# Performance work log

Measured on AMD Instinct MI355X. Metric: run time of the kernel, lower is better.

## Reference

```python
import jax, jax.numpy as jnp
import numpy as np

D = 2048; HQ = 16; HKV = 4; HD = 128
E = 8; F = 2048; FS = 11008; TOPK = 2
B = 2; S = 1024
EPS = 1e-6
NEG = -1e9


def setup_inputs() -> dict:
    key = jax.random.key(0)
    ks = jax.random.split(key, 16)
    p = lambda k, shape: jax.random.normal(k, shape, jnp.float32) * 0.02
    # rotary tables (rotate-half convention): [S, HD]
    pos = jnp.arange(S, dtype=jnp.float32)[:, None]
    inv = 1.0 / (10000.0 ** (jnp.arange(0, HD, 2, dtype=jnp.float32) / HD))
    ang = pos * inv[None, :]
    cos = jnp.concatenate([jnp.cos(ang), jnp.cos(ang)], axis=-1)
    sin = jnp.concatenate([jnp.sin(ang), jnp.sin(ang)], axis=-1)
    return dict(
        x=jax.random.normal(ks[0], (B, S, D), jnp.float32),
        rope_cos=cos, rope_sin=sin,
        attn_norm_w=jnp.ones((D,), jnp.float32),
        ffn_norm_w=jnp.ones((D,), jnp.float32),
        wq=p(ks[1], (D, HQ * HD)), bq=jnp.zeros((HQ * HD,), jnp.float32),
        wk=p(ks[2], (D, HKV * HD)), bk=jnp.zeros((HKV * HD,), jnp.float32),
        wv=p(ks[3], (D, HKV * HD)), bv=jnp.zeros((HKV * HD,), jnp.float32),
        wo=p(ks[4], (HQ * HD, D)),
        router_w=p(ks[5], (D, E)),
        w_gate=p(ks[6], (E, D, F)), w_up=p(ks[7], (E, D, F)), w_down=p(ks[8], (E, F, D)),
        ws_gate=p(ks[9], (D, FS)), ws_up=p(ks[10], (D, FS)), ws_down=p(ks[11], (FS, D)),
    )


def rmsnorm(x, w):
    return x * jax.lax.rsqrt(jnp.mean(x * x, axis=-1, keepdims=True) + EPS) * w


def rotate_half(x):
    x1, x2 = jnp.split(x, 2, axis=-1)
    return jnp.concatenate([-x2, x1], axis=-1)


def reference(x, rope_cos, rope_sin, attn_norm_w, ffn_norm_w,
              wq, bq, wk, bk, wv, bv, wo, router_w,
              w_gate, w_up, w_down, ws_gate, ws_up, ws_down):
    b, s, d = x.shape
    # ---- attention sublayer ----
    h = rmsnorm(x, attn_norm_w)
    q = (h @ wq + bq).reshape(b, s, HQ, HD)
    k = (h @ wk + bk).reshape(b, s, HKV, HD)
    v = (h @ wv + bv).reshape(b, s, HKV, HD)
    cos = rope_cos[None, :, None, :]
    sin = rope_sin[None, :, None, :]
    q = q * cos + rotate_half(q) * sin
    k = k * cos + rotate_half(k) * sin
    rep = HQ // HKV
    k = jnp.repeat(k, rep, axis=2)   # [b,s,HQ,HD]
    v = jnp.repeat(v, rep, axis=2)
    scores = jnp.einsum('bqhd,bkhd->bhqk', q, k) / np.sqrt(HD).astype(np.float32)
    causal = jnp.tril(jnp.ones((s, s), bool))
    scores = jnp.where(causal[None, None], scores, NEG)
    attn = jax.nn.softmax(scores, axis=-1)
    o = jnp.einsum('bhqk,bkhd->bqhd', attn, v).reshape(b, s, HQ * HD) @ wo
    new_k, new_v = k, v
    x = x + o
    # ---- MoE sublayer ----
    hn = rmsnorm(x, ffn_norm_w).reshape(b * s, d)   # [T,D]
    logits = hn @ router_w                           # [T,E]
    probs = jax.nn.softmax(logits, axis=-1)
    topv, topi = jax.lax.top_k(probs, TOPK)          # [T,K]
    topv = topv / jnp.sum(topv, axis=-1, keepdims=True)
    onehot = jax.nn.one_hot(topi, E, dtype=hn.dtype)  # [T,K,E]
    wdense = jnp.einsum('tke,tk->te', onehot, topv)   # sparse combine weights [T,E]
    g = jnp.einsum('td,edf->tef', hn, w_gate)
    u = jnp.einsum('td,edf->tef', hn, w_up)
    y = jnp.einsum('tef,efd->ted', jax.nn.silu(g) * u, w_down)
    routed = jnp.einsum('ted,te->td', y, wdense)
    shared = (jax.nn.silu(hn @ ws_gate) * (hn @ ws_up)) @ ws_down
    moe = (routed + shared).reshape(b, s, d)
    # load-balancing aux loss (Switch/Mixtral convention)
    frac = jnp.mean(onehot, axis=(0, 1))             # fraction dispatched per expert
    pmean = jnp.mean(probs, axis=0)
    aux_loss = E * jnp.sum(frac * pmean)
    out = x + moe
    return out, (new_k, new_v), aux_loss
```

## Files before the change

### kernel.cpp

```cpp
#include <hip/hip_runtime.h>

typedef unsigned short u16;
typedef unsigned int u32;
typedef unsigned long long u64;
typedef __attribute__((ext_vector_type(4))) unsigned short u16x4;
typedef __attribute__((ext_vector_type(8))) unsigned short u16x8;
typedef __attribute__((ext_vector_type(4))) float f32x4;
typedef __attribute__((ext_vector_type(8))) __bf16 bf16x8;

#define DD 2048
#define TT 2048
#define FSH 11008

__device__ __forceinline__ float bf2f(u16 u) {
  union { u32 i; float f; } v; v.i = ((u32)u) << 16; return v.f;
}
__device__ __forceinline__ u16 f2bf(float f) {
  union { float f; u32 i; } v; v.f = f;
  u32 r = v.i + 0x7fffu + ((v.i >> 16) & 1u);
  return (u16)(r >> 16);
}
__device__ __forceinline__ void gld16(const void* g, void* l) {
  __builtin_amdgcn_global_load_lds((const __attribute__((address_space(1))) void*)g,
                                   (__attribute__((address_space(3))) void*)l, 16, 0, 0);
}

#define MFMA16(d, a, b) d = __builtin_amdgcn_mfma_f32_16x16x32_bf16(a, b, d, 0, 0, 0)

__global__ __launch_bounds__(256) void rmsnorm_k(const float* __restrict__ x,
                                                 const float* __restrict__ w,
                                                 u16* __restrict__ out) {
  const int t = threadIdx.x;
  const float* xr = x + (size_t)blockIdx.x * DD;
  float4 a = *(const float4*)(xr + t * 8);
  float4 b = *(const float4*)(xr + t * 8 + 4);
  float ss = a.x*a.x + a.y*a.y + a.z*a.z + a.w*a.w
           + b.x*b.x + b.y*b.y + b.z*b.z + b.w*b.w;
#pragma unroll
  for (int m = 1; m < 64; m <<= 1) ss += __shfl_xor(ss, m);
  __shared__ float red[4];
  if ((t & 63) == 0) red[t >> 6] = ss;
  __syncthreads();
  float sc = rsqrtf((red[0] + red[1] + red[2] + red[3]) * (1.f / DD) + 1e-6f);
  float4 wa = *(const float4*)(w + t * 8);
  float4 wb = *(const float4*)(w + t * 8 + 4);
  u16x8 o;
  o[0] = f2bf(a.x * sc * wa.x); o[1] = f2bf(a.y * sc * wa.y);
  o[2] = f2bf(a.z * sc * wa.z); o[3] = f2bf(a.w * sc * wa.w);
  o[4] = f2bf(b.x * sc * wb.x); o[5] = f2bf(b.y * sc * wb.y);
  o[6] = f2bf(b.z * sc * wb.z); o[7] = f2bf(b.w * sc * wb.w);
  *(u16x8*)(out + (size_t)blockIdx.x * DD + t * 8) = o;
}

__global__ __launch_bounds__(256) void transp_k(const float* __restrict__ W,
                                                u16* __restrict__ Wt, int R, int C) {
  __shared__ u16 tile[64 * 80];
  const size_t msz = (size_t)R * C;
  const float* Wm = W + msz * blockIdx.z;
  u16* Wtm = Wt + msz * blockIdx.z;
  const int t = threadIdx.x;
  const int n0 = blockIdx.x * 64, k0 = blockIdx.y * 64;
#pragma unroll
  for (int p = 0; p < 4; ++p) {
    const int kk = (t >> 4) + p * 16;
    const int nn = (t & 15) * 4;
    float4 v = *(const float4*)(Wm + (size_t)(k0 + kk) * C + n0 + nn);
    const float vv[4] = {v.x, v.y, v.z, v.w};
#pragma unroll
    for (int j = 0; j < 4; ++j) {
      const int n = nn + j;
      tile[n * 80 + (kk ^ (((n >> 2) & 7) << 3))] = f2bf(vv[j]);
    }
  }
  __syncthreads();
#pragma unroll
  for (int p = 0; p < 2; ++p) {
    const int n = (t >> 3) + p * 32;
    const int c = t & 7;
    u16x8 v = *(const u16x8*)(tile + n * 80 + ((c * 8) ^ (((n >> 2) & 7) << 3)));
    *(u16x8*)(Wtm + (size_t)(n0 + n) * R + k0 + c * 8) = v;
  }
}

template <int EPI, bool EXPERT, bool INDIR, bool SPLITK>
__global__ __launch_bounds__(256) void gemm2(
    const u16* __restrict__ A, const u16* __restrict__ Bt, void* __restrict__ Cp,
    const void* __restrict__ aux, const float* __restrict__ slotw,
    const int* __restrict__ slot_tok, const int* __restrict__ tiletab,
    int M, int N, int K, int Kc) {
  __shared__ u16 lA[128 * 32];
  __shared__ u16 lB[128 * 32];
  const int t = threadIdx.x, w = t >> 6, l = t & 63;
  const int n0 = blockIdx.x * 128;
  int m0;
  if constexpr (EXPERT) {
    const int ntil = tiletab[0];
    if ((int)blockIdx.y >= ntil) return;
    const int e = tiletab[1 + blockIdx.y * 2];
    m0 = tiletab[2 + blockIdx.y * 2];
    Bt += (size_t)e * N * K;
  } else {
    m0 = blockIdx.y * 128;
  }
  int kbase = 0, KC = K;
  if constexpr (SPLITK) { kbase = blockIdx.z * Kc; KC = Kc; }
  const int srow = w * 16 + (l >> 2);
  const int scol = (l & 3) * 8;
  const int r0 = m0 + srow, r1 = m0 + srow + 64;
  const u16 *ag0, *ag1;
  if constexpr (INDIR) {
    ag0 = A + (size_t)slot_tok[r0] * K + scol + kbase;
    ag1 = A + (size_t)slot_tok[r1] * K + scol + kbase;
  } else {
    ag0 = A + (size_t)r0 * K + scol + kbase;
    ag1 = A + (size_t)r1 * K + scol + kbase;
  }
  const u16* bg0 = Bt + (size_t)(n0 + srow) * K + scol + kbase;
  const u16* bg1 = Bt + (size_t)(n0 + srow + 64) * K + scol + kbase;
  u16* la = lA + w * 512;
  u16* lb = lB + w * 512;
  const int l15 = l & 15, l4 = l >> 4;
  const int wm = w >> 1, wn = w & 1;
  const int fa = (wm * 64 + l15) * 32 + l4 * 8;
  const int fb = (wn * 64 + l15) * 32 + l4 * 8;
  f32x4 acc[4][4] = {};
  for (int ko = 0; ko < KC; ko += 32) {
    __syncthreads();
    gld16(ag0 + ko, la);
    gld16(ag1 + ko, la + 2048);
    gld16(bg0 + ko, lb);
    gld16(bg1 + ko, lb + 2048);
    asm volatile("s_waitcnt vmcnt(0)" ::: "memory");
    __syncthreads();
    bf16x8 af[4], bf[4];
#pragma unroll
    for (int i = 0; i < 4; ++i) {
      af[i] = *(const bf16x8*)(lA + fa + i * 512);
      bf[i] = *(const bf16x8*)(lB + fb + i * 512);
    }
#pragma unroll
    for (int mi = 0; mi < 4; ++mi)
#pragma unroll
      for (int ni = 0; ni < 4; ++ni)
        MFMA16(acc[mi][ni], af[mi], bf[ni]);
  }
  float* Cf = (float*)Cp;
  if constexpr (SPLITK) Cf += (size_t)blockIdx.z * M * N;
#pragma unroll
  for (int mi = 0; mi < 4; ++mi) {
#pragma unroll
    for (int r = 0; r < 4; ++r) {
      const int row = m0 + wm * 64 + mi * 16 + l4 * 4 + r;
#pragma unroll
      for (int ni = 0; ni < 4; ++ni) {
        const int col = n0 + wn * 64 + ni * 16 + l15;
        const size_t idx = (size_t)row * N + col;
        const float v = acc[mi][ni][r];
        if constexpr (EPI == 0) Cf[idx] = v;
        else if constexpr (EPI == 2) ((u16*)Cp)[idx] = f2bf(v);
        else if constexpr (EPI == 3) {
          const float g = bf2f(((const u16*)aux)[idx]);
          ((u16*)Cp)[idx] = f2bf(v * g / (1.f + __expf(-g)));
        } else {
          ((u16*)Cp)[idx] = f2bf(slotw[row] * v);
        }
      }
    }
  }
}

__global__ __launch_bounds__(512) void gemm2gu(
    const u16* __restrict__ A, const u16* __restrict__ Btg, const u16* __restrict__ Btu,
    u16* __restrict__ act, const int* __restrict__ slot_tok, const int* __restrict__ tiletab,
    int N, int K, int ebase) {
  __shared__ u16 SH[16384];
  const int t = threadIdx.x, w = t >> 6, l = t & 63;
  const int n0 = blockIdx.x * 128;
  const int ntil = tiletab[0];
  if ((int)blockIdx.y >= ntil) return;
  const int e = tiletab[1 + blockIdx.y * 2];
  if (e < ebase || e >= ebase + 4) return;
  const int m0 = tiletab[2 + blockIdx.y * 2];
  const size_t boff = (size_t)(e - ebase) * N * K;
  const u16* Bg = Btg + boff;
  const u16* Bu = Btu + boff;
  const int srow = w * 16 + (l >> 2);
  const int scol = (l & 3) * 8;
  const u16* ag = A + (size_t)slot_tok[m0 + srow] * K + scol;
  const u16* bgp = Bg + (size_t)(n0 + srow) * K + scol;
  const u16* bup = Bu + (size_t)(n0 + srow) * K + scol;
  u16* la = SH + w * 512;
  u16* lbg = SH + 4096 + w * 512;
  u16* lbu = SH + 8192 + w * 512;
  const int l15 = l & 15, l4 = l >> 4;
  const int wm = w >> 2, wn = w & 3;
  const int mat = wn >> 1, ch = wn & 1;
  const int fa = (wm * 64 + l15) * 32 + l4 * 8;
  const int fb = (mat ? 8192 : 4096) + (ch * 64 + l15) * 32 + l4 * 8;
  f32x4 acc[4][4] = {};
  for (int ko = 0; ko < K; ko += 32) {
    __syncthreads();
    gld16(ag + ko, la);
    gld16(bgp + ko, lbg);
    gld16(bup + ko, lbu);
    asm volatile("s_waitcnt vmcnt(0)" ::: "memory");
    __syncthreads();
    bf16x8 af[4], bf[4];
#pragma unroll
    for (int i = 0; i < 4; ++i) {
      af[i] = *(const bf16x8*)(SH + fa + i * 512);
      bf[i] = *(const bf16x8*)(SH + fb + i * 512);
    }
#pragma unroll
    for (int mi = 0; mi < 4; ++mi)
#pragma unroll
      for (int ni = 0; ni < 4; ++ni)
        MFMA16(acc[mi][ni], af[mi], bf[ni]);
  }
  __syncthreads();
  if (mat == 0) {
    u16* gr = SH + (wm * 2 + ch) * 4096;
#pragma unroll
    for (int mi = 0; mi < 4; ++mi)
#pragma unroll
      for (int r = 0; r < 4; ++r)
#pragma unroll
        for (int ni = 0; ni < 4; ++ni)
          gr[(mi * 16 + l4 * 4 + r) * 64 + ni * 16 + l15] = f2bf(acc[mi][ni][r]);
  }
  __syncthreads();
  if (mat == 1) {
    const u16* gr = SH + (wm * 2 + ch) * 4096;
#pragma unroll
    for (int mi = 0; mi < 4; ++mi)
#pragma unroll
      for (int r = 0; r < 4; ++r) {
        const int row = m0 + wm * 64 + mi * 16 + l4 * 4 + r;
#pragma unroll
        for (int ni = 0; ni < 4; ++ni) {
          const float g = bf2f(gr[(mi * 16 + l4 * 4 + r) * 64 + ni * 16 + l15]);
          const float u = acc[mi][ni][r];
          act[(size_t)row * N + n0 + ch * 64 + ni * 16 + l15] =
              f2bf(u * g / (1.f + __expf(-g)));
        }
      }
  }
}

template <int EPI, bool SPLITK>
__global__ __launch_bounds__(512, 2) void gemm8(
    const u16* __restrict__ A, const u16* __restrict__ Bt, void* __restrict__ Cp,
    const u16* __restrict__ aux, int M, int N, int K, int Kc) {
  __shared__ char lds[131072];
  const int t = threadIdx.x, w = t >> 6, l = t & 63;
  const int gx = gridDim.x, gy = gridDim.y;
  const int nwg = gx * gy;
  int wg = blockIdx.y * gx + blockIdx.x;
  wg = (wg & 7) * (nwg >> 3) + (wg >> 3);
  const int m0 = (wg % gy) * 256;
  const int n0 = (wg / gy) * 256;
  int kbase = 0, KC = K;
  if constexpr (SPLITK) {
    kbase = blockIdx.z * Kc;
    const int rem = K - kbase;
    KC = rem < Kc ? rem : Kc;
  }
  const int ktiles = KC >> 6;
  const int wm = w >> 2, wn = w & 3;
  const int l15 = l & 15, l4 = l >> 4;
  const int sro = l >> 3, sc = l & 7;

  const u16* sgp[2][2][2];
  u32 sdo[2][2][2];
#pragma unroll
  for (int isB = 0; isB < 2; ++isB)
#pragma unroll
    for (int h = 0; h < 2; ++h)
#pragma unroll
      for (int i = 0; i < 2; ++i) {
        const int q = i * 8 + w;
        const int r0 = isB ? (((q >> 2) << 6) + h * 32 + (q & 3) * 8)
                           : (((q & 8) << 4) + h * 64 + (q & 7) * 8);
        const int r = r0 + sro;
        const int cl = sc ^ (r & 7);
        const u16* base = isB ? (Bt + (size_t)(n0 + r) * K) : (A + (size_t)(m0 + r) * K);
        sgp[isB][h][i] = base + kbase + cl * 8;
        sdo[isB][h][i] = (u32)(isB * 32768 + r0 * 128);
      }
  auto stage = [&](int b, int isB, int h, int kt) {
    const int kk = kt < ktiles ? kt : ktiles - 1;
#pragma unroll
    for (int i = 0; i < 2; ++i)
      gld16(sgp[isB][h][i] + kk * 64, lds + b * 65536 + sdo[isB][h][i]);
  };
  auto ldA = [&](int b, int mi, int ks) {
    const int row = wm * 128 + mi * 16 + l15;
    const int ch = (ks * 4 + l4) ^ (row & 7);
    return *(const bf16x8*)(lds + b * 65536 + row * 128 + ch * 16);
  };
  auto ldB = [&](int b, int ni, int ks) {
    const int row = wn * 64 + ni * 16 + l15;
    const int ch = (ks * 4 + l4) ^ (row & 7);
    return *(const bf16x8*)(lds + b * 65536 + 32768 + row * 128 + ch * 16);
  };

  f32x4 acc[8][4] = {};
  bf16x8 aR[4][2], b0[2][2], b1[2][2];

  stage(0, 0, 0, 0); stage(0, 1, 0, 0); stage(0, 1, 1, 0); stage(0, 0, 1, 0);
  stage(1, 0, 0, 1); stage(1, 1, 1, 1); stage(1, 0, 1, 1);
  asm volatile("s_waitcnt vmcnt(6)" ::: "memory");
  __builtin_amdgcn_s_barrier();

  for (int kt = 0; kt < ktiles; kt += 2) {
#pragma unroll
    for (int mi = 0; mi < 4; ++mi) { aR[mi][0] = ldA(0, mi, 0); aR[mi][1] = ldA(0, mi, 1); }
#pragma unroll
    for (int ni = 0; ni < 2; ++ni) { b0[ni][0] = ldB(0, ni, 0); b0[ni][1] = ldB(0, ni, 1); }
    stage(1, 1, 0, kt + 1);
    __builtin_amdgcn_s_barrier();
    asm volatile("s_waitcnt lgkmcnt(0)" ::: "memory");
    __builtin_amdgcn_s_setprio(1);
#pragma unroll
    for (int mi = 0; mi < 4; ++mi)
#pragma unroll
      for (int ni = 0; ni < 2; ++ni) {
        MFMA16(acc[mi][ni], aR[mi][0], b0[ni][0]);
        MFMA16(acc[mi][ni], aR[mi][1], b0[ni][1]);
      }
    __builtin_amdgcn_s_setprio(0);
    __builtin_amdgcn_s_barrier();
#pragma unroll
    for (int ni = 0; ni < 2; ++ni) { b1[ni][0] = ldB(0, ni + 2, 0); b1[ni][1] = ldB(0, ni + 2, 1); }
    stage(0, 0, 0, kt + 2);
    __builtin_amdgcn_s_barrier();
    asm volatile("s_waitcnt lgkmcnt(0)" ::: "memory");
    __builtin_amdgcn_s_setprio(1);
#pragma unroll
    for (int mi = 0; mi < 4; ++mi)
#pragma unroll
      for (int ni = 0; ni < 2; ++ni) {
        MFMA16(acc[mi][ni + 2], aR[mi][0], b1[ni][0]);
        MFMA16(acc[mi][ni + 2], aR[mi][1], b1[ni][1]);
// ... 29 lines not shown
    asm volatile("s_waitcnt vmcnt(6)" ::: "memory");
    __builtin_amdgcn_s_barrier();
#pragma unroll
    for (int mi = 0; mi < 4; ++mi) { aR[mi][0] = ldA(1, mi, 0); aR[mi][1] = ldA(1, mi, 1); }
#pragma unroll
    for (int ni = 0; ni < 2; ++ni) { b0[ni][0] = ldB(1, ni, 0); b0[ni][1] = ldB(1, ni, 1); }
    stage(0, 1, 0, kt + 2);
    __builtin_amdgcn_s_barrier();
    asm volatile("s_waitcnt lgkmcnt(0)" ::: "memory");
    __builtin_amdgcn_s_setprio(1);
#pragma unroll
    for (int mi = 0; mi < 4; ++mi)
#pragma unroll
      for (int ni = 0; ni < 2; ++ni) {
        MFMA16(acc[mi][ni], aR[mi][0], b0[ni][0]);
        MFMA16(acc[mi][ni], aR[mi][1], b0[ni][1]);
      }
    __builtin_amdgcn_s_setprio(0);
    __builtin_amdgcn_s_barrier();
#pragma unroll
    for (int ni = 0; ni < 2; ++ni) { b1[ni][0] = ldB(1, ni + 2, 0); b1[ni][1] = ldB(1, ni + 2, 1); }
    stage(1, 0, 0, kt + 3);
    __builtin_amdgcn_s_barrier();
    asm volatile("s_waitcnt lgkmcnt(0)" ::: "memory");
    __builtin_amdgcn_s_setprio(1);
#pragma unroll
    for (int mi = 0; mi < 4; ++mi)
#pragma unroll
      for (int ni = 0; ni < 2; ++ni) {
        MFMA16(acc[mi][ni + 2], aR[mi][0], b1[ni][0]);
        MFMA16(acc[mi][ni + 2], aR[mi][1], b1[ni][1]);
      }
    __builtin_amdgcn_s_setprio(0);
    __builtin_amdgcn_s_barrier();
#pragma unroll
    for (int mi = 0; mi < 4; ++mi) { aR[mi][0] = ldA(1, mi + 4, 0); aR[mi][1] = ldA(1, mi + 4, 1); }
    stage(1, 1, 1, kt + 3);
    __builtin_amdgcn_s_barrier();
    asm volatile("s_waitcnt lgkmcnt(0)" ::: "memory");
    __builtin_amdgcn_s_setprio(1);
#pragma unroll
    for (int mi = 0; mi < 4; ++mi)
#pragma unroll
      for (int ni = 0; ni < 2; ++ni) {
        MFMA16(acc[mi + 4][ni + 2], aR[mi][0], b1[ni][0]);
        MFMA16(acc[mi + 4][ni + 2], aR[mi][1], b1[ni][1]);
      }
    __builtin_amdgcn_s_setprio(0);
    __builtin_amdgcn_s_barrier();
    stage(1, 0, 1, kt + 3);
    __builtin_amdgcn_s_barrier();
    __builtin_amdgcn_s_setprio(1);
#pragma unroll
    for (int mi = 0; mi < 4; ++mi)
#pragma unroll
      for (int ni = 0; ni < 2; ++ni) {
        MFMA16(acc[mi + 4][ni], aR[mi][0], b0[ni][0]);
        MFMA16(acc[mi + 4][ni], aR[mi][1], b0[ni][1]);
      }
    __builtin_amdgcn_s_setprio(0);
    asm volatile("s_waitcnt vmcnt(6)" ::: "memory");
    __builtin_amdgcn_s_barrier();
  }

  u16* C16 = (u16*)Cp;
  float* Cf = (float*)Cp;
  if constexpr (EPI == 10) C16 += (size_t)blockIdx.z * ((size_t)M * N);
  if constexpr (EPI == 11) Cf += (size_t)blockIdx.z * ((size_t)M * N);
#pragma unroll
  for (int mi = 0; mi < 8; ++mi)
#pragma unroll
    for (int rr = 0; rr < 4; ++rr) {
      const int row = m0 + wm * 128 + mi * 16 + l4 * 4 + rr;
#pragma unroll
      for (int ni = 0; ni < 4; ++ni) {
        const int col = n0 + wn * 64 + ni * 16 + l15;
        const size_t idx = (size_t)row * N + col;
        const float v = acc[mi][ni][rr];
        if constexpr (EPI == 11) {
          Cf[idx] = v;
        } else if constexpr (EPI == 3) {
          const float g = bf2f(aux[idx]);
          C16[idx] = f2bf(v * g / (1.f + __expf(-g)));
        } else {
          C16[idx] = f2bf(v);
        }
      }
    }
}

__global__ __launch_bounds__(512, 2) void gemm_gu(
    const u16* __restrict__ A, const u16* __restrict__ Btg, const u16* __restrict__ Btu,
    u16* __restrict__ act, int K, int LDC, int cg0) {
  __shared__ char lds[131072];
  const int t = threadIdx.x, w = t >> 6, l = t & 63;
  const int gx = gridDim.x;
  const int nwg = gx * 8;
  int wg = blockIdx.y * gx + blockIdx.x;
  wg = (wg & 7) * (nwg >> 3) + (wg >> 3);
  const int m0 = (wg & 7) * 256;
  const int nt = wg >> 3;
  const int ktiles = K >> 6;
  const int wm = w >> 2, wn = w & 3;
  const int l15 = l & 15, l4 = l >> 4;
  const int sro = l >> 3, sc = l & 7;

  const u16* sga[2][2]; u32 sda[2][2];
#pragma unroll
  for (int h = 0; h < 2; ++h)
#pragma unroll
    for (int i = 0; i < 2; ++i) {
      const int q = i * 8 + w;
      const int r0 = ((q & 8) << 4) + h * 64 + (q & 7) * 8;
      const int r = r0 + sro;
      const int cl = sc ^ (r & 7);
      sga[h][i] = A + (size_t)(m0 + r) * K + cl * 8;
      sda[h][i] = (u32)(r0 * 128);
    }
  const u16* sgb[2][2]; u32 sdb[2][2];
#pragma unroll
  for (int mat = 0; mat < 2; ++mat)
#pragma unroll
    for (int i = 0; i < 2; ++i) {
      const int q = i * 8 + w;
      const int r0 = q * 8;
      const int r = r0 + sro;
      const int cl = sc ^ (r & 7);
      const u16* B = mat ? Btu : Btg;
      sgb[mat][i] = B + (size_t)(nt * 128 + r) * K + cl * 8;
      sdb[mat][i] = (u32)(32768 + mat * 16384 + r0 * 128);
    }
  auto stgA = [&](int b, int h, int kt) {
    const int kk = kt < ktiles ? kt : ktiles - 1;
#pragma unroll
    for (int i = 0; i < 2; ++i) gld16(sga[h][i] + kk * 64, lds + b * 65536 + sda[h][i]);
  };
  auto stgB = [&](int b, int mat, int kt) {
    const int kk = kt < ktiles ? kt : ktiles - 1;
#pragma unroll
    for (int i = 0; i < 2; ++i) gld16(sgb[mat][i] + kk * 64, lds + b * 65536 + sdb[mat][i]);
  };
  auto ldA = [&](int b, int mi, int ks) {
    const int row = wm * 128 + mi * 16 + l15;
    const int ch = (ks * 4 + l4) ^ (row & 7);
    return *(const bf16x8*)(lds + b * 65536 + row * 128 + ch * 16);
  };
  auto ldB = [&](int b, int mat, int ni, int ks) {
    const int row = wn * 32 + ni * 16 + l15;
    const int ch = (ks * 4 + l4) ^ (row & 7);
    return *(const bf16x8*)(lds + b * 65536 + 32768 + mat * 16384 + row * 128 + ch * 16);
  };

  f32x4 accg[8][2] = {}, accu[8][2] = {};
  bf16x8 aR[4][2], bg[2][2], bu[2][2];

  stgA(0, 0, 0); stgB(0, 0, 0); stgB(0, 1, 0); stgA(0, 1, 0);
  stgA(1, 0, 1); stgB(1, 1, 1); stgA(1, 1, 1);
  asm volatile("s_waitcnt vmcnt(6)" ::: "memory");
  __builtin_amdgcn_s_barrier();

  for (int kt = 0; kt < ktiles; kt += 2) {
#pragma unroll
    for (int mi = 0; mi < 4; ++mi) { aR[mi][0] = ldA(0, mi, 0); aR[mi][1] = ldA(0, mi, 1); }
#pragma unroll
    for (int ni = 0; ni < 2; ++ni) { bg[ni][0] = ldB(0, 0, ni, 0); bg[ni][1] = ldB(0, 0, ni, 1); }
    stgB(1, 0, kt + 1);
    __builtin_amdgcn_s_barrier();
    asm volatile("s_waitcnt lgkmcnt(0)" ::: "memory");
    __builtin_amdgcn_s_setprio(1);
#pragma unroll
    for (int mi = 0; mi < 4; ++mi)
#pragma unroll
      for (int ni = 0; ni < 2; ++ni) {
        MFMA16(accg[mi][ni], aR[mi][0], bg[ni][0]);
        MFMA16(accg[mi][ni], aR[mi][1], bg[ni][1]);
      }
    __builtin_amdgcn_s_setprio(0);
    __builtin_amdgcn_s_barrier();
#pragma unroll
    for (int ni = 0; ni < 2; ++ni) { bu[ni][0] = ldB(0, 1, ni, 0); bu[ni][1] = ldB(0, 1, ni, 1); }
    stgA(0, 0, kt + 2);
    __builtin_amdgcn_s_barrier();
    asm volatile("s_waitcnt lgkmcnt(0)" ::: "memory");
    __builtin_amdgcn_s_setprio(1);
#pragma unroll
    for (int mi = 0; mi < 4; ++mi)
#pragma unroll
      for (int ni = 0; ni < 2; ++ni) {
        MFMA16(accu[mi][ni], aR[mi][0], bu[ni][0]);
        MFMA16(accu[mi][ni], aR[mi][1], bu[ni][1]);
      }
    __builtin_amdgcn_s_setprio(0);
    __builtin_amdgcn_s_barrier();
#pragma unroll
    for (int mi = 0; mi < 4; ++mi) { aR[mi][0] = ldA(0, mi + 4, 0); aR[mi][1] = ldA(0, mi + 4, 1); }
    stgB(0, 1, kt + 2);
    __builtin_amdgcn_s_barrier();
    asm volatile("s_waitcnt lgkmcnt(0)" ::: "memory");
    __builtin_amdgcn_s_setprio(1);
#pragma unroll
    for (int mi = 0; mi < 4; ++mi)
#pragma unroll
      for (int ni = 0; ni < 2; ++ni) {
        MFMA16(accu[mi + 4][ni], aR[mi][0], bu[ni][0]);
        MFMA16(accu[mi + 4][ni], aR[mi][1], bu[ni][1]);
      }
    __builtin_amdgcn_s_setprio(0);
    __builtin_amdgcn_s_barrier();
    stgA(0, 1, kt + 2);
    __builtin_amdgcn_s_barrier();
    __builtin_amdgcn_s_setprio(1);
// ... 288 lines not shown
  const size_t base = (size_t)tok * DD + t * 8;
  float v[8];
  {
    float4 a = *(const float4*)(x + base);
    float4 b = *(const float4*)(x + base + 4);
    v[0] = a.x; v[1] = a.y; v[2] = a.z; v[3] = a.w;
    v[4] = b.x; v[5] = b.y; v[6] = b.z; v[7] = b.w;
  }
#pragma unroll
  for (int p = 0; p < 4; ++p) {
    const float* pr = parts + (size_t)p * (TT * DD) + base;
    float4 a = *(const float4*)(pr);
    float4 b = *(const float4*)(pr + 4);
    v[0] += a.x; v[1] += a.y; v[2] += a.z; v[3] += a.w;
    v[4] += b.x; v[5] += b.y; v[6] += b.z; v[7] += b.w;
  }
  *(float4*)(X2 + base) = make_float4(v[0], v[1], v[2], v[3]);
  *(float4*)(X2 + base + 4) = make_float4(v[4], v[5], v[6], v[7]);
  float ss = 0.f;
#pragma unroll
  for (int j = 0; j < 8; ++j) ss += v[j] * v[j];
#pragma unroll
  for (int m = 1; m < 64; m <<= 1) ss += __shfl_xor(ss, m);
  __shared__ float red[4];
  __shared__ float racc[32];
  if ((t & 63) == 0) red[w] = ss;
  __syncthreads();
  const float sc = rsqrtf((red[0] + red[1] + red[2] + red[3]) * (1.f / DD) + 1e-6f);
  float hn[8];
  u16x8 o;
#pragma unroll
  for (int j = 0; j < 8; ++j) {
    hn[j] = v[j] * sc * wn[t * 8 + j];
    o[j] = f2bf(hn[j]);
  }
  *(u16x8*)(HN + base) = o;
  float acc[8] = {};
#pragma unroll
  for (int j = 0; j < 8; ++j) {
    const int d = t * 8 + j;
    float4 r0 = *(const float4*)(rw + d * 8);
    float4 r1 = *(const float4*)(rw + d * 8 + 4);
    acc[0] += hn[j] * r0.x; acc[1] += hn[j] * r0.y; acc[2] += hn[j] * r0.z; acc[3] += hn[j] * r0.w;
    acc[4] += hn[j] * r1.x; acc[5] += hn[j] * r1.y; acc[6] += hn[j] * r1.z; acc[7] += hn[j] * r1.w;
  }
#pragma unroll
  for (int m = 1; m < 64; m <<= 1)
#pragma unroll
    for (int e = 0; e < 8; ++e) acc[e] += __shfl_xor(acc[e], m);
  if ((t & 63) == 0)
#pragma unroll
    for (int e = 0; e < 8; ++e) racc[w * 8 + e] = acc[e];
  __syncthreads();
  if (t == 0) {
    float lg[8];
#pragma unroll
    for (int e = 0; e < 8; ++e) lg[e] = racc[e] + racc[8 + e] + racc[16 + e] + racc[24 + e];
    float mx = lg[0];
#pragma unroll
    for (int e = 1; e < 8; ++e) mx = fmaxf(mx, lg[e]);
    float p[8], sum = 0.f;
#pragma unroll
    for (int e = 0; e < 8; ++e) { p[e] = __expf(lg[e] - mx); sum += p[e]; }
    const float inv = 1.f / sum;
#pragma unroll
    for (int e = 0; e < 8; ++e) p[e] *= inv;
    *(float4*)(probs + tok * 8) = make_float4(p[0], p[1], p[2], p[3]);
    *(float4*)(probs + tok * 8 + 4) = make_float4(p[4], p[5], p[6], p[7]);
    int e0 = 0; float v0 = p[0];
#pragma unroll
    for (int e = 1; e < 8; ++e) if (p[e] > v0) { v0 = p[e]; e0 = e; }
    int e1 = (e0 == 0) ? 1 : 0; float v1 = p[e1];
#pragma unroll
    for (int e = 0; e < 8; ++e) if (e != e0 && p[e] > v1) { v1 = p[e]; e1 = e; }
    const float wsum = v0 + v1;
    topi2[tok * 2] = e0; topi2[tok * 2 + 1] = e1;
    topw2[tok * 2] = v0 / wsum; topw2[tok * 2 + 1] = v1 / wsum;
  }
}

__global__ __launch_bounds__(256) void zero_k(int* __restrict__ slot_tok,
                                              float* __restrict__ slot_w) {
  const int i = blockIdx.x * 256 + threadIdx.x;
  if (i < 5120) { slot_tok[i] = 0; slot_w[i] = 0.f; }
}

__global__ __launch_bounds__(256) void scan2_k(const int* __restrict__ topi2,
                                               const float* __restrict__ probs,
                                               int* __restrict__ cursors,
                                               int* __restrict__ tiletab,
                                               float* __restrict__ auxout) {
  const int t = threadIdx.x, w = t >> 6, l = t & 63;
  __shared__ int cnt[8];
  __shared__ float wsum[4][8];
  if (t < 8) cnt[t] = 0;
  __syncthreads();
  float ps[8] = {};
  for (int i = t; i < 2048; i += 256) {
    atomicAdd(&cnt[topi2[i * 2]], 1);
    atomicAdd(&cnt[topi2[i * 2 + 1]], 1);
    float4 a = *(const float4*)(probs + i * 8);
    float4 b = *(const float4*)(probs + i * 8 + 4);
    ps[0] += a.x; ps[1] += a.y; ps[2] += a.z; ps[3] += a.w;
    ps[4] += b.x; ps[5] += b.y; ps[6] += b.z; ps[7] += b.w;
  }
#pragma unroll
  for (int m = 1; m < 64; m <<= 1)
#pragma unroll
    for (int e = 0; e < 8; ++e) ps[e] += __shfl_xor(ps[e], m);
  if (l == 0)
#pragma unroll
    for (int e = 0; e < 8; ++e) wsum[w][e] = ps[e];
  __syncthreads();
  if (t == 0) {
    int off = 0, nt = 0;
    float aux = 0.f;
    for (int e = 0; e < 8; ++e) {
      cursors[e] = off;
      const int c = cnt[e];
      const int nte = (c + 127) >> 7;
      for (int i = 0; i < nte; ++i) {
        tiletab[1 + nt * 2] = e;
        tiletab[2 + nt * 2] = off + i * 128;
        ++nt;
      }
      off += nte * 128;
      const float pm = (wsum[0][e] + wsum[1][e] + wsum[2][e] + wsum[3][e]) * (1.f / 2048.f);
      aux += ((float)c * (1.f / 4096.f)) * pm;
    }
    tiletab[0] = nt;
    *auxout = 8.f * aux;
  }
}

__global__ __launch_bounds__(256) void assign_k(const int* __restrict__ topi2,
                                                const float* __restrict__ topw2,
                                                int* __restrict__ cursors,
                                                int* __restrict__ slot_tok,
                                                float* __restrict__ slot_w,
                                                int* __restrict__ tok_slot) {
  __shared__ int lcnt[8];
  __shared__ int base[8];
  const int t = threadIdx.x;
  const int tok = blockIdx.x * 256 + t;
  if (t < 8) lcnt[t] = 0;
  __syncthreads();
  int e[2], lr[2];
#pragma unroll
  for (int j = 0; j < 2; ++j) {
    e[j] = topi2[tok * 2 + j];
    lr[j] = atomicAdd(&lcnt[e[j]], 1);
  }
  __syncthreads();
  if (t < 8) base[t] = atomicAdd(&cursors[t], lcnt[t]);
  __syncthreads();
#pragma unroll
  for (int j = 0; j < 2; ++j) {
    const int s = base[e[j]] + lr[j];
    slot_tok[s] = tok;
    slot_w[s] = topw2[tok * 2 + j];
    tok_slot[tok * 2 + j] = s;
  }
}

__global__ __launch_bounds__(256) void final_k(float* __restrict__ out,
                                               const u16* __restrict__ routed,
                                               const int* __restrict__ tok_slot) {
  const int tok = blockIdx.x, t = threadIdx.x;
  const int s0 = tok_slot[tok * 2], s1 = tok_slot[tok * 2 + 1];
  u16x8 a = ((const u16x8*)(routed + (size_t)s0 * DD))[t];
  u16x8 b = ((const u16x8*)(routed + (size_t)s1 * DD))[t];
  float* o = out + (size_t)tok * DD + t * 8;
  float4 o0 = *(const float4*)o;
  float4 o1 = *(const float4*)(o + 4);
  o0.x += bf2f(a[0]) + bf2f(b[0]); o0.y += bf2f(a[1]) + bf2f(b[1]);
  o0.z += bf2f(a[2]) + bf2f(b[2]); o0.w += bf2f(a[3]) + bf2f(b[3]);
  o1.x += bf2f(a[4]) + bf2f(b[4]); o1.y += bf2f(a[5]) + bf2f(b[5]);
  o1.z += bf2f(a[6]) + bf2f(b[6]); o1.w += bf2f(a[7]) + bf2f(b[7]);
  *(float4*)o = o0;
  *(float4*)(o + 4) = o1;
}

extern "C" void kernel_launch(void* const* d_in, const int* in_sizes, int n_in,
                              void* d_out, int out_size, void* d_ws, size_t ws_size,
                              hipStream_t stream) {
  (void)in_sizes; (void)n_in; (void)out_size; (void)ws_size;
  const float* x    = (const float*)d_in[0];
  const float* rc   = (const float*)d_in[1];
  const float* rs   = (const float*)d_in[2];
  const float* anw  = (const float*)d_in[3];
  const float* fnw  = (const float*)d_in[4];
  const float* wq   = (const float*)d_in[5];
  const float* bq   = (const float*)d_in[6];
  const float* wk   = (const float*)d_in[7];
  const float* bk   = (const float*)d_in[8];
  const float* wv   = (const float*)d_in[9];
  const float* bv   = (const float*)d_in[10];
  const float* wo   = (const float*)d_in[11];
  const float* rw   = (const float*)d_in[12];
  const float* wg   = (const float*)d_in[13];
  const float* wu   = (const float*)d_in[14];
  const float* wd   = (const float*)d_in[15];
  const float* wsg  = (const float*)d_in[16];
  const float* wsu  = (const float*)d_in[17];
  const float* wsd  = (const float*)d_in[18];

  const size_t MB = (size_t)1 << 20;
  char* ws = (char*)d_ws;
  float* X2  = (float*)(ws + 0);
  u16*   HN  = (u16*)(ws + 16 * MB);
  char*  SM  = ws + 24 * MB;
  char*  AR  = ws + 25 * MB;

  int*   CURS  = (int*)(SM + 256);
  int*   TILT  = (int*)(SM + 512);
  int*   TOPI  = (int*)(SM + 4096);
  float* TOPW  = (float*)(SM + 40960);
  int*   STOK  = (int*)(SM + 73728);
  float* SW    = (float*)(SM + 98304);
  int*   TSLOT = (int*)(SM + 131072);
  float* PROBS = (float*)(SM + 163840);

  u16*   H      = (u16*)(AR);
  u16*   WTQ    = (u16*)(AR + 8 * MB);
  u16*   PARTSQ = (u16*)(AR + 20 * MB);
  u16*   ATTNO = (u16*)(AR);
  u16*   QR    = (u16*)(AR + 68 * MB);
  u16*   KR    = (u16*)(AR + 76 * MB);
  u16*   VBb   = (u16*)(AR + 78 * MB);
  u16*   WTO    = (u16*)(AR + 8 * MB);
  float* PARTSW = (float*)(AR + 16 * MB);
  u16*   G      = (u16*)(AR);
  u16*   WTSg   = (u16*)(AR + 43 * MB);
  u16*   WTSu   = (u16*)(AR + 59 * MB);
  u16*   WTSd   = (u16*)(AR + 43 * MB);
  u16*   PARTSD = (u16*)(AR + 86 * MB);
  u16*   WTEg   = (u16*)(AR);
  u16*   WTEu   = (u16*)(AR + 32 * MB);
  u16*   ACT    = (u16*)(AR + 64 * MB);
  u16*   ROUTED = (u16*)(AR + 84 * MB);
  u16*   WTEd   = (u16*)(AR);

  float* out  = (float*)d_out;
  float* NK   = out + 4194304;
  float* NV   = out + 2 * 4194304;
  float* AUXO = out + 3 * 4194304;

  const dim3 b256(256);
  const dim3 b512(512);

  rmsnorm_k<<<TT, b256, 0, stream>>>(x, anw, H);
  transp_k<<<dim3(32, 32, 1), b256, 0, stream>>>(wq, WTQ, 2048, 2048);
  transp_k<<<dim3(8, 32, 1), b256, 0, stream>>>(wk, WTQ + (size_t)2048 * 2048, 2048, 512);
  transp_k<<<dim3(8, 32, 1), b256, 0, stream>>>(wv, WTQ + (size_t)2560 * 2048, 2048, 512);
  gemm8<10, true><<<dim3(12, 8, 2), b512, 0, stream>>>(H, WTQ, PARTSQ, nullptr, TT, 3072, 2048, 1024);
  rope_k<<<dim3(1024, 2), b256, 0, stream>>>(PARTSQ, PARTSQ + (size_t)TT * 3072, rc, rs,
                                             bq, bk, bv, QR, KR, VBb, NK, NV);
  attn_k<<<dim3(16, 16, 2), b256, 0, stream>>>(QR, KR, VBb, ATTNO);
  transp_k<<<dim3(32, 32, 1), b256, 0, stream>>>(wo, WTO, 2048, 2048);
  gemm8<11, true><<<dim3(8, 8, 4), b512, 0, stream>>>(ATTNO, WTO, PARTSW, nullptr, TT, 2048, 2048, 512);
  zero_k<<<20, b256, 0, stream>>>(STOK, SW);
  fuserouter_k<<<TT, b256, 0, stream>>>(x, PARTSW, fnw, rw, X2, HN, TOPI, TOPW, PROBS);
  scan2_k<<<1, b256, 0, stream>>>(TOPI, PROBS, CURS, TILT, AUXO);
  assign_k<<<8, b256, 0, stream>>>(TOPI, TOPW, CURS, STOK, SW, TSLOT);
  {
    const int cg[4] = {0, 3712, 7424, 11008};
    for (int gi = 0; gi < 3; ++gi) {
      const int c0 = cg[gi], wgrp = cg[gi + 1] - c0, ngc = wgrp >> 7;
      transp_k<<<dim3(wgrp / 64, 32, 1), b256, 0, stream>>>(wsg + c0, WTSg, 2048, FSH);
      transp_k<<<dim3(wgrp / 64, 32, 1), b256, 0, stream>>>(wsu + c0, WTSu, 2048, FSH);
      gemm_gu<<<dim3(ngc, 8, 1), b512, 0, stream>>>(HN, WTSg, WTSu, G, 2048, FSH, c0);
    }
  }
  transp_k<<<dim3(32, 172, 1), b256, 0, stream>>>(wsd, WTSd, FSH, 2048);
  gemm8<10, true><<<dim3(8, 8, 4), b512, 0, stream>>>(G, WTSd, PARTSD, nullptr, TT, 2048, FSH, 2816);
  redbf_k<<<2048, b256, 0, stream>>>(out, X2, PARTSD);
  for (int cb = 0; cb < 2; ++cb) {
    const int eb = cb * 4;
    transp_k<<<dim3(32, 32, 4), b256, 0, stream>>>(wg + (size_t)eb * 2048 * 2048, WTEg, 2048, 2048);
    transp_k<<<dim3(32, 32, 4), b256, 0, stream>>>(wu + (size_t)eb * 2048 * 2048, WTEu, 2048, 2048);
    gemm2gu<<<dim3(16, 40, 1), b512, 0, stream>>>(HN, WTEg, WTEu, ACT, STOK, TILT, 2048, 2048, eb);
  }
  transp_k<<<dim3(32, 32, 8), b256, 0, stream>>>(wd, WTEd, 2048, 2048);
  gemm2<4, true, false, false><<<dim3(16, 40, 1), b256, 0, stream>>>(
      ACT, WTEd, ROUTED, nullptr, SW, STOK, TILT, 5120, 2048, 2048, 0);
  final_k<<<TT, b256, 0, stream>>>(out, ROUTED, TSLOT);
}
```

Measured before the change: 906.9 us.

## Route MoE expert GEMMs through the large-tile gemm8/gemm_gu kernels with 256-row tiles

Removes the simple 128x128 expert kernels (gemm2, gemm2gu) and adds an EXPERT mode to the tuned 256x256 gemm8 and gemm_gu kernels, which use a 128KB LDS pipeline. Expert row tiles grow from 128 to 256 slots, so the tile table, slot buffers and zeroing are resized to match (6144 slots). The larger tiles should give more data reuse and better MFMA throughput. The cost is more padding waste per expert and fewer workgroups when expert token counts are uneven.

```diff
diff --git a/kernel.cpp b/kernel.cpp
--- a/kernel.cpp
+++ b/kernel.cpp
@@ -82,183 +82,29 @@
   }
 }
 
-template <int EPI, bool EXPERT, bool INDIR, bool SPLITK>
-__global__ __launch_bounds__(256) void gemm2(
+template <int EPI, bool SPLITK, bool EXPERT>
+__global__ __launch_bounds__(512, 2) void gemm8(
     const u16* __restrict__ A, const u16* __restrict__ Bt, void* __restrict__ Cp,
-    const void* __restrict__ aux, const float* __restrict__ slotw,
-    const int* __restrict__ slot_tok, const int* __restrict__ tiletab,
-    int M, int N, int K, int Kc) {
-  __shared__ u16 lA[128 * 32];
-  __shared__ u16 lB[128 * 32];
+    const u16* __restrict__ aux, const float* __restrict__ slotw,
+    const int* __restrict__ tiletab, int M, int N, int K, int Kc) {
+  __shared__ char lds[131072];
   const int t = threadIdx.x, w = t >> 6, l = t & 63;
-  const int n0 = blockIdx.x * 128;
-  int m0;
+  int m0, n0;
   if constexpr (EXPERT) {
     const int ntil = tiletab[0];
     if ((int)blockIdx.y >= ntil) return;
     const int e = tiletab[1 + blockIdx.y * 2];
     m0 = tiletab[2 + blockIdx.y * 2];
+    n0 = blockIdx.x * 256;
     Bt += (size_t)e * N * K;
   } else {
-    m0 = blockIdx.y * 128;
-  }
-  int kbase = 0, KC = K;
-  if constexpr (SPLITK) { kbase = blockIdx.z * Kc; KC = Kc; }
-  const int srow = w * 16 + (l >> 2);
-  const int scol = (l & 3) * 8;
-  const int r0 = m0 + srow, r1 = m0 + srow + 64;
-  const u16 *ag0, *ag1;
-  if constexpr (INDIR) {
-    ag0 = A + (size_t)slot_tok[r0] * K + scol + kbase;
-    ag1 = A + (size_t)slot_tok[r1] * K + scol + kbase;
-  } else {
-    ag0 = A + (size_t)r0 * K + scol + kbase;
-    ag1 = A + (size_t)r1 * K + scol + kbase;
-  }
-  const u16* bg0 = Bt + (size_t)(n0 + srow) * K + scol + kbase;
-  const u16* bg1 = Bt + (size_t)(n0 + srow + 64) * K + scol + kbase;
-  u16* la = lA + w * 512;
-  u16* lb = lB + w * 512;
-  const int l15 = l & 15, l4 = l >> 4;
-  const int wm = w >> 1, wn = w & 1;
-  const int fa = (wm * 64 + l15) * 32 + l4 * 8;
-  const int fb = (wn * 64 + l15) * 32 + l4 * 8;
-  f32x4 acc[4][4] = {};
-  for (int ko = 0; ko < KC; ko += 32) {
-    __syncthreads();
-    gld16(ag0 + ko, la);
-    gld16(ag1 + ko, la + 2048);
-    gld16(bg0 + ko, lb);
-    gld16(bg1 + ko, lb + 2048);
-    asm volatile("s_waitcnt vmcnt(0)" ::: "memory");
-    __syncthreads();
-    bf16x8 af[4], bf[4];
-#pragma unroll
-    for (int i = 0; i < 4; ++i) {
-      af[i] = *(const bf16x8*)(lA + fa + i * 512);
-      bf[i] = *(const bf16x8*)(lB + fb + i * 512);
-    }
-#pragma unroll
-    for (int mi = 0; mi < 4; ++mi)
-#pragma unroll
-      for (int ni = 0; ni < 4; ++ni)
-        MFMA16(acc[mi][ni], af[mi], bf[ni]);
-  }
-  float* Cf = (float*)Cp;
-  if constexpr (SPLITK) Cf += (size_t)blockIdx.z * M * N;
-#pragma unroll
-  for (int mi = 0; mi < 4; ++mi) {
-#pragma unroll
-    for (int r = 0; r < 4; ++r) {
-      const int row = m0 + wm * 64 + mi * 16 + l4 * 4 + r;
-#pragma unroll
-      for (int ni = 0; ni < 4; ++ni) {
-        const int col = n0 + wn * 64 + ni * 16 + l15;
-        const size_t idx = (size_t)row * N + col;
-        const float v = acc[mi][ni][r];
-        if constexpr (EPI == 0) Cf[idx] = v;
-        else if constexpr (EPI == 2) ((u16*)Cp)[idx] = f2bf(v);
-        else if constexpr (EPI == 3) {
-          const float g = bf2f(((const u16*)aux)[idx]);
-          ((u16*)Cp)[idx] = f2bf(v * g / (1.f + __expf(-g)));
-        } else {
-          ((u16*)Cp)[idx] = f2bf(slotw[row] * v);
-        }
-      }
-    }
-  }
-}
-
-__global__ __launch_bounds__(512) void gemm2gu(
-    const u16* __restrict__ A, const u16* __restrict__ Btg, const u16* __restrict__ Btu,
-    u16* __restrict__ act, const int* __restrict__ slot_tok, const int* __restrict__ tiletab,
-    int N, int K, int ebase) {
-  __shared__ u16 SH[16384];
-  const int t = threadIdx.x, w = t >> 6, l = t & 63;
-  const int n0 = blockIdx.x * 128;
-  const int ntil = tiletab[0];
-  if ((int)blockIdx.y >= ntil) return;
-  const int e = tiletab[1 + blockIdx.y * 2];
-  if (e < ebase || e >= ebase + 4) return;
-  const int m0 = tiletab[2 + blockIdx.y * 2];
-  const size_t boff = (size_t)(e - ebase) * N * K;
-  const u16* Bg = Btg + boff;
-  const u16* Bu = Btu + boff;
-  const int srow = w * 16 + (l >> 2);
-  const int scol = (l & 3) * 8;
-  const u16* ag = A + (size_t)slot_tok[m0 + srow] * K + scol;
-  const u16* bgp = Bg + (size_t)(n0 + srow) * K + scol;
-  const u16* bup = Bu + (size_t)(n0 + srow) * K + scol;
-  u16* la = SH + w * 512;
-  u16* lbg = SH + 4096 + w * 512;
-  u16* lbu = SH + 8192 + w * 512;
-  const int l15 = l & 15, l4 = l >> 4;
-  const int wm = w >> 2, wn = w & 3;
-  const int mat = wn >> 1, ch = wn & 1;
-  const int fa = (wm * 64 + l15) * 32 + l4 * 8;
-  const int fb = (mat ? 8192 : 4096) + (ch * 64 + l15) * 32 + l4 * 8;
-  f32x4 acc[4][4] = {};
-  for (int ko = 0; ko < K; ko += 32) {
-    __syncthreads();
-    gld16(ag + ko, la);
-    gld16(bgp + ko, lbg);
-    gld16(bup + ko, lbu);
-    asm volatile("s_waitcnt vmcnt(0)" ::: "memory");
-    __syncthreads();
-    bf16x8 af[4], bf[4];
-#pragma unroll
-    for (int i = 0; i < 4; ++i) {
-      af[i] = *(const bf16x8*)(SH + fa + i * 512);
-      bf[i] = *(const bf16x8*)(SH + fb + i * 512);
-    }
-#pragma unroll
-    for (int mi = 0; mi < 4; ++mi)
-#pragma unroll
-      for (int ni = 0; ni < 4; ++ni)
-        MFMA16(acc[mi][ni], af[mi], bf[ni]);
-  }
-  __syncthreads();
-  if (mat == 0) {
-    u16* gr = SH + (wm * 2 + ch) * 4096;
-#pragma unroll
-    for (int mi = 0; mi < 4; ++mi)
-#pragma unroll
-      for (int r = 0; r < 4; ++r)
-#pragma unroll
-        for (int ni = 0; ni < 4; ++ni)
-          gr[(mi * 16 + l4 * 4 + r) * 64 + ni * 16 + l15] = f2bf(acc[mi][ni][r]);
-  }
-  __syncthreads();
-  if (mat == 1) {
-    const u16* gr = SH + (wm * 2 + ch) * 4096;
-#pragma unroll
-    for (int mi = 0; mi < 4; ++mi)
-#pragma unroll
-      for (int r = 0; r < 4; ++r) {
-        const int row = m0 + wm * 64 + mi * 16 + l4 * 4 + r;
-#pragma unroll
-        for (int ni = 0; ni < 4; ++ni) {
-          const float g = bf2f(gr[(mi * 16 + l4 * 4 + r) * 64 + ni * 16 + l15]);
-          const float u = acc[mi][ni][r];
-          act[(size_t)row * N + n0 + ch * 64 + ni * 16 + l15] =
-              f2bf(u * g / (1.f + __expf(-g)));
-        }
-      }
-  }
-}
-
-template <int EPI, bool SPLITK>
-__global__ __launch_bounds__(512, 2) void gemm8(
-    const u16* __restrict__ A, const u16* __restrict__ Bt, void* __restrict__ Cp,
-    const u16* __restrict__ aux, int M, int N, int K, int Kc) {
-  __shared__ char lds[131072];
-  const int t = threadIdx.x, w = t >> 6, l = t & 63;
-  const int gx = gridDim.x, gy = gridDim.y;
-  const int nwg = gx * gy;
-  int wg = blockIdx.y * gx + blockIdx.x;
-  wg = (wg & 7) * (nwg >> 3) + (wg >> 3);
-  const int m0 = (wg % gy) * 256;
-  const int n0 = (wg / gy) * 256;
+    const int gx = gridDim.x, gy = gridDim.y;
+    const int nwg = gx * gy;
+    int wg = blockIdx.y * gx + blockIdx.x;
+    wg = (wg & 7) * (nwg >> 3) + (wg >> 3);
+    m0 = (wg % gy) * 256;
+    n0 = (wg / gy) * 256;
+  }
   int kbase = 0, KC = K;
   if constexpr (SPLITK) {
     kbase = blockIdx.z * Kc;
@@ -454,6 +300,8 @@
         } else if constexpr (EPI == 3) {
           const float g = bf2f(aux[idx]);
           C16[idx] = f2bf(v * g / (1.f + __expf(-g)));
+        } else if constexpr (EPI == 4) {
+          C16[idx] = f2bf(slotw[row] * v);
         } else {
           C16[idx] = f2bf(v);
         }
@@ -461,17 +309,35 @@
     }
 }
 
+template <bool EXPERT>
 __global__ __launch_bounds__(512, 2) void gemm_gu(
     const u16* __restrict__ A, const u16* __restrict__ Btg, const u16* __restrict__ Btu,
-    u16* __restrict__ act, int K, int LDC, int cg0) {
+    u16* __restrict__ act, const int* __restrict__ slot_tok, const int* __restrict__ tiletab,
+    int K, int LDC, int cg0, int ebase) {
   __shared__ char lds[131072];
   const int t = threadIdx.x, w = t >> 6, l = t & 63;
-  const int gx = gridDim.x;
-  const int nwg = gx * 8;
-  int wg = blockIdx.y * gx + blockIdx.x;
-  wg = (wg & 7) * (nwg >> 3) + (wg >> 3);
-  const int m0 = (wg & 7) * 256;
-  const int nt = wg >> 3;
+  int m0, nt;
+  const u16 *Bg, *Bu;
+  if constexpr (EXPERT) {
+    const int ntil = tiletab[0];
+    if ((int)blockIdx.y >= ntil) return;
+    const int e = tiletab[1 + blockIdx.y * 2];
+    if (e < ebase || e >= ebase + 4) return;
+    m0 = tiletab[2 + blockIdx.y * 2];
+    nt = blockIdx.x;
+    const size_t boff = (size_t)(e - ebase) * LDC * K;
+    Bg = Btg + boff;
+    Bu = Btu + boff;
+  } else {
+    const int gx = gridDim.x;
+    const int nwg = gx * 8;
+    int wg = blockIdx.y * gx + blockIdx.x;
+    wg = (wg & 7) * (nwg >> 3) + (wg >> 3);
+    m0 = (wg & 7) * 256;
+    nt = wg >> 3;
+    Bg = Btg;
+    Bu = Btu;
+  }
   const int ktiles = K >> 6;
   const int wm = w >> 2, wn = w & 3;
   const int l15 = l & 15, l4 = l >> 4;
@@ -486,7 +352,10 @@
       const int r0 = ((q & 8) << 4) + h * 64 + (q & 7) * 8;
       const int r = r0 + sro;
       const int cl = sc ^ (r & 7);
-      sga[h][i] = A + (size_t)(m0 + r) * K + cl * 8;
+      size_t arow;
+      if constexpr (EXPERT) arow = (size_t)slot_tok[m0 + r];
+      else arow = (size_t)(m0 + r);
+      sga[h][i] = A + arow * K + cl * 8;
       sda[h][i] = (u32)(r0 * 128);
     }
   const u16* sgb[2][2]; u32 sdb[2][2];
@@ -498,7 +367,7 @@
       const int r0 = q * 8;
       const int r = r0 + sro;
       const int cl = sc ^ (r & 7);
-      const u16* B = mat ? Btu : Btg;
+      const u16* B = mat ? Bu : Bg;
       sgb[mat][i] = B + (size_t)(nt * 128 + r) * K + cl * 8;
       sdb[mat][i] = (u32)(32768 + mat * 16384 + r0 * 128);
     }
@@ -953,7 +822,7 @@
 __global__ __launch_bounds__(256) void zero_k(int* __restrict__ slot_tok,
                                               float* __restrict__ slot_w) {
   const int i = blockIdx.x * 256 + threadIdx.x;
-  if (i < 5120) { slot_tok[i] = 0; slot_w[i] = 0.f; }
+  if (i < 6144) { slot_tok[i] = 0; slot_w[i] = 0.f; }
 }
 
 __global__ __launch_bounds__(256) void scan2_k(const int* __restrict__ topi2,
@@ -989,13 +858,13 @@
     for (int e = 0; e < 8; ++e) {
       cursors[e] = off;
       const int c = cnt[e];
-      const int nte = (c + 127) >> 7;
+      const int nte = (c + 255) >> 8;
       for (int i = 0; i < nte; ++i) {
         tiletab[1 + nt * 2] = e;
-        tiletab[2 + nt * 2] = off + i * 128;
+        tiletab[2 + nt * 2] = off + i * 256;
         ++nt;
       }
-      off += nte * 128;
+      off += nte * 256;
       const float pm = (wsum[0][e] + wsum[1][e] + wsum[2][e] + wsum[3][e]) * (1.f / 2048.f);
       aux += ((float)c * (1.f / 4096.f)) * pm;
     }
@@ -1108,9 +977,9 @@
   u16*   PARTSD = (u16*)(AR + 86 * MB);
   u16*   WTEg   = (u16*)(AR);
   u16*   WTEu   = (u16*)(AR + 32 * MB);
+  u16*   WTEd   = (u16*)(AR);
   u16*   ACT    = (u16*)(AR + 64 * MB);
-  u16*   ROUTED = (u16*)(AR + 84 * MB);
-  u16*   WTEd   = (u16*)(AR);
+  u16*   ROUTED = (u16*)(AR + 88 * MB);
 
   float* out  = (float*)d_out;
   float* NK   = out + 4194304;
@@ -1124,13 +993,15 @@
   transp_k<<<dim3(32, 32, 1), b256, 0, stream>>>(wq, WTQ, 2048, 2048);
   transp_k<<<dim3(8, 32, 1), b256, 0, stream>>>(wk, WTQ + (size_t)2048 * 2048, 2048, 512);
   transp_k<<<dim3(8, 32, 1), b256, 0, stream>>>(wv, WTQ + (size_t)2560 * 2048, 2048, 512);
-  gemm8<10, true><<<dim3(12, 8, 2), b512, 0, stream>>>(H, WTQ, PARTSQ, nullptr, TT, 3072, 2048, 1024);
+  gemm8<10, true, false><<<dim3(12, 8, 2), b512, 0, stream>>>(
+      H, WTQ, PARTSQ, nullptr, nullptr, nullptr, TT, 3072, 2048, 1024);
   rope_k<<<dim3(1024, 2), b256, 0, stream>>>(PARTSQ, PARTSQ + (size_t)TT * 3072, rc, rs,
                                              bq, bk, bv, QR, KR, VBb, NK, NV);
   attn_k<<<dim3(16, 16, 2), b256, 0, stream>>>(QR, KR, VBb, ATTNO);
   transp_k<<<dim3(32, 32, 1), b256, 0, stream>>>(wo, WTO, 2048, 2048);
-  gemm8<11, true><<<dim3(8, 8, 4), b512, 0, stream>>>(ATTNO, WTO, PARTSW, nullptr, TT, 2048, 2048, 512);
-  zero_k<<<20, b256, 0, stream>>>(STOK, SW);
+  gemm8<11, true, false><<<dim3(8, 8, 4), b512, 0, stream>>>(
+      ATTNO, WTO, PARTSW, nullptr, nullptr, nullptr, TT, 2048, 2048, 512);
+  zero_k<<<24, b256, 0, stream>>>(STOK, SW);
   fuserouter_k<<<TT, b256, 0, stream>>>(x, PARTSW, fnw, rw, X2, HN, TOPI, TOPW, PROBS);
   scan2_k<<<1, b256, 0, stream>>>(TOPI, PROBS, CURS, TILT, AUXO);
   assign_k<<<8, b256, 0, stream>>>(TOPI, TOPW, CURS, STOK, SW, TSLOT);
@@ -1140,20 +1011,23 @@
       const int c0 = cg[gi], wgrp = cg[gi + 1] - c0, ngc = wgrp >> 7;
       transp_k<<<dim3(wgrp / 64, 32, 1), b256, 0, stream>>>(wsg + c0, WTSg, 2048, FSH);
       transp_k<<<dim3(wgrp / 64, 32, 1), b256, 0, stream>>>(wsu + c0, WTSu, 2048, FSH);
-      gemm_gu<<<dim3(ngc, 8, 1), b512, 0, stream>>>(HN, WTSg, WTSu, G, 2048, FSH, c0);
+      gemm_gu<false><<<dim3(ngc, 8, 1), b512, 0, stream>>>(
+          HN, WTSg, WTSu, G, nullptr, nullptr, 2048, FSH, c0, 0);
     }
   }
   transp_k<<<dim3(32, 172, 1), b256, 0, stream>>>(wsd, WTSd, FSH, 2048);
-  gemm8<10, true><<<dim3(8, 8, 4), b512, 0, stream>>>(G, WTSd, PARTSD, nullptr, TT, 2048, FSH, 2816);
+  gemm8<10, true, false><<<dim3(8, 8, 4), b512, 0, stream>>>(
+      G, WTSd, PARTSD, nullptr, nullptr, nullptr, TT, 2048, FSH, 2816);
   redbf_k<<<2048, b256, 0, stream>>>(out, X2, PARTSD);
   for (int cb = 0; cb < 2; ++cb) {
     const int eb = cb * 4;
     transp_k<<<dim3(32, 32, 4), b256, 0, stream>>>(wg + (size_t)eb * 2048 * 2048, WTEg, 2048, 2048);
     transp_k<<<dim3(32, 32, 4), b256, 0, stream>>>(wu + (size_t)eb * 2048 * 2048, WTEu, 2048, 2048);
-    gemm2gu<<<dim3(16, 40, 1), b512, 0, stream>>>(HN, WTEg, WTEu, ACT, STOK, TILT, 2048, 2048, eb);
+    gemm_gu<true><<<dim3(16, 24, 1), b512, 0, stream>>>(
+        HN, WTEg, WTEu, ACT, STOK, TILT, 2048, 2048, 0, eb);
   }
   transp_k<<<dim3(32, 32, 8), b256, 0, stream>>>(wd, WTEd, 2048, 2048);
-  gemm2<4, true, false, false><<<dim3(16, 40, 1), b256, 0, stream>>>(
-      ACT, WTEd, ROUTED, nullptr, SW, STOK, TILT, 5120, 2048, 2048, 0);
+  gemm8<4, false, true><<<dim3(8, 24, 1), b512, 0, stream>>>(
+      ACT, WTEd, ROUTED, nullptr, SW, TILT, 0, 2048, 2048, 0);
   final_k<<<TT, b256, 0, stream>>>(out, ROUTED, TSLOT);
 }
```

Measured after the change: 851.6 us. -6.1%, faster.
